# Kernel tuning notes

Measured on AMD Instinct MI355X. Metric: run time of the kernel, lower is better.

Reference implementation:

```python
import jax, jax.numpy as jnp
import numpy as np

N, S, IN_F, TEXT_D, EMB, H = 128, 1024, 768, 512, 512, 8
HD = EMB // H  # 64


def setup_inputs() -> dict:
    key = jax.random.key(0)
    ks = jax.random.split(key, 14)
    sc = 0.02
    return {
        "v": jax.random.normal(ks[0], (1, N, 12, IN_F), dtype=jnp.float32),
        "t": jax.random.normal(ks[1], (N, S, TEXT_D), dtype=jnp.float32),
        "t_len": jax.random.randint(ks[2], (N,), 1, S + 1, dtype=jnp.int32),
        "W_fc1": jax.random.normal(ks[3], (EMB, IN_F), dtype=jnp.float32) * sc,
        "b_fc1": jnp.zeros((EMB,), jnp.float32),
        "W_fc2": jax.random.normal(ks[4], (EMB, 12 * EMB), dtype=jnp.float32) * sc,
        "b_fc2": jnp.zeros((EMB,), jnp.float32),
        "Wq": jax.random.normal(ks[5], (EMB, EMB), dtype=jnp.float32) * sc,
        "Wk": jax.random.normal(ks[6], (EMB, TEXT_D), dtype=jnp.float32) * sc,
        "Wv": jax.random.normal(ks[7], (EMB, TEXT_D), dtype=jnp.float32) * sc,
        "bq": jnp.zeros((EMB,), jnp.float32),
        "bk": jnp.zeros((EMB,), jnp.float32),
        "bv": jnp.zeros((EMB,), jnp.float32),
        "Wo": jax.random.normal(ks[8], (EMB, EMB), dtype=jnp.float32) * sc,
        "bo": jnp.zeros((EMB,), jnp.float32),
    }


def reference(v, t, t_len, W_fc1, b_fc1, W_fc2, b_fc2, Wq, Wk, Wv, bq, bk, bv, Wo, bo):
    # fc1 + ReLU: [1,N,12,IN_F] -> [N,12,EMB]
    x = jax.nn.relu(jnp.einsum('onif,ef->onie', v, W_fc1) + b_fc1)[0]
    # flatten + fc2 + ReLU -> [N, EMB]
    x = x.reshape(N, 12 * EMB)
    vfeat = jax.nn.relu(x @ W_fc2.T + b_fc2)
    # Batched ragged multihead attention, query length 1 per item.
    scale = 1.0 / jnp.sqrt(jnp.asarray(HD, vfeat.dtype))
    q = ((vfeat @ Wq.T + bq) * scale).reshape(N, H, HD)           # [N,H,HD]
    k = (jnp.einsum('nsd,ed->nse', t, Wk) + bk).reshape(N, S, H, HD)
    vv = (jnp.einsum('nsd,ed->nse', t, Wv) + bv).reshape(N, S, H, HD)
    scores = jnp.einsum('nhd,nshd->nhs', q, k)                    # [N,H,S]
    valid = (jnp.arange(S)[None, :] < t_len[:, None])[:, None, :]  # [N,1,S]
    scores = jnp.where(valid, scores, jnp.finfo(scores.dtype).min)
    w = jax.nn.softmax(scores, axis=-1)                           # [N,H,S]
    ctx = jnp.einsum('nhs,nshd->nhd', w, vv).reshape(N, EMB)
    attn_out = ctx @ Wo.T + bo                                    # [N,EMB]
    return vfeat, attn_out
```

## Files before the change

### kernel.cpp

```cpp
#include <hip/hip_runtime.h>

#define NB 128
#define SSEQ 1024
#define TD 512
#define TSTR 516

typedef _Float16 half8 __attribute__((ext_vector_type(8)));
typedef _Float16 half4 __attribute__((ext_vector_type(4)));
typedef float f32x4 __attribute__((ext_vector_type(4)));

template<int AM, int BM>
__device__ __forceinline__ void gemm_body(
    const void* __restrict__ Av, int lda, long aSZ,
    const void* __restrict__ Bv, int ldb, long bSZ,
    const float* __restrict__ bias, const float* __restrict__ aRowScale,
    float scale, int doRelu, int outMode,
    float* __restrict__ outF, _Float16* __restrict__ outH,
    int ldc, int cColOff, int kTiles, long oSplit,
    int mt, int nt, int sp, int bz, int tid)
{
  __shared__ _Float16 As[64][72];
  __shared__ _Float16 Bs[64][72];
  int r = tid >> 2, kq = (tid & 3) * 16;
  int w = tid >> 6, l = tid & 63;
  long aoff = (long)bz * aSZ + (long)(mt * 64 + r) * lda + (long)sp * kTiles * 64 + kq;
  long boff = (long)bz * bSZ + (long)(nt * 64 + r) * ldb + (long)sp * kTiles * 64 + kq;
  const _Float16* apH = (const _Float16*)Av + aoff;
  const float*    apF = (const float*)Av + aoff;
  const _Float16* bpH = (const _Float16*)Bv + boff;
  const float*    bpF = (const float*)Bv + boff;
  float srA = 1.0f;
  if constexpr (AM == 2) srA = 1.0f / aRowScale[(mt * 64 + r) * 8 + bz];

  half8 pa0, pa1, pb0, pb1;
  f32x4 qa0, qa1, qa2, qa3, qc0, qc1, qc2, qc3;
  if constexpr (AM == 0) { pa0 = *(const half8*)apH; pa1 = *(const half8*)(apH + 8); }
  else { qa0 = *(const f32x4*)apF; qa1 = *(const f32x4*)(apF + 4);
         qa2 = *(const f32x4*)(apF + 8); qa3 = *(const f32x4*)(apF + 12); }
  if constexpr (BM == 0) { pb0 = *(const half8*)bpH; pb1 = *(const half8*)(bpH + 8); }
  else { qc0 = *(const f32x4*)bpF; qc1 = *(const f32x4*)(bpF + 4);
         qc2 = *(const f32x4*)(bpF + 8); qc3 = *(const f32x4*)(bpF + 12); }

  f32x4 acc[4];
  #pragma unroll
  for (int c = 0; c < 4; ++c) acc[c] = (f32x4){0.f, 0.f, 0.f, 0.f};
  int fr = l & 15, fo = (l >> 4) * 8;
  for (int kt = 0; kt < kTiles; ++kt) {
    __syncthreads();
    if constexpr (AM == 0) {
      *(half8*)&As[r][kq] = pa0; *(half8*)&As[r][kq + 8] = pa1;
    } else {
      f32x4 s0 = qa0, s1 = qa1, s2 = qa2, s3 = qa3;
      if constexpr (AM == 2) { s0 *= srA; s1 *= srA; s2 *= srA; s3 *= srA; }
      *(half4*)&As[r][kq + 0]  = __builtin_convertvector(s0, half4);
      *(half4*)&As[r][kq + 4]  = __builtin_convertvector(s1, half4);
      *(half4*)&As[r][kq + 8]  = __builtin_convertvector(s2, half4);
      *(half4*)&As[r][kq + 12] = __builtin_convertvector(s3, half4);
    }
    if constexpr (BM == 0) {
      *(half8*)&Bs[r][kq] = pb0; *(half8*)&Bs[r][kq + 8] = pb1;
    } else {
      *(half4*)&Bs[r][kq + 0]  = __builtin_convertvector(qc0, half4);
      *(half4*)&Bs[r][kq + 4]  = __builtin_convertvector(qc1, half4);
      *(half4*)&Bs[r][kq + 8]  = __builtin_convertvector(qc2, half4);
      *(half4*)&Bs[r][kq + 12] = __builtin_convertvector(qc3, half4);
    }
    __syncthreads();
    if (kt + 1 < kTiles) {
      apH += 64; apF += 64; bpH += 64; bpF += 64;
      if constexpr (AM == 0) { pa0 = *(const half8*)apH; pa1 = *(const half8*)(apH + 8); }
      else { qa0 = *(const f32x4*)apF; qa1 = *(const f32x4*)(apF + 4);
             qa2 = *(const f32x4*)(apF + 8); qa3 = *(const f32x4*)(apF + 12); }
      if constexpr (BM == 0) { pb0 = *(const half8*)bpH; pb1 = *(const half8*)(bpH + 8); }
      else { qc0 = *(const f32x4*)bpF; qc1 = *(const f32x4*)(bpF + 4);
             qc2 = *(const f32x4*)(bpF + 8); qc3 = *(const f32x4*)(bpF + 12); }
    }
    #pragma unroll
    for (int ks = 0; ks < 2; ++ks) {
      half8 af = *(const half8*)&As[16 * w + fr][ks * 32 + fo];
      #pragma unroll
      for (int c = 0; c < 4; ++c) {
        half8 bf = *(const half8*)&Bs[16 * c + fr][ks * 32 + fo];
        acc[c] = __builtin_amdgcn_mfma_f32_16x16x32_f16(af, bf, acc[c], 0, 0, 0);
      }
    }
  }
  int lrow = (l >> 4) * 4, lcol = l & 15;
  #pragma unroll
  for (int c = 0; c < 4; ++c) {
    #pragma unroll
    for (int rr = 0; rr < 4; ++rr) {
      int gm = mt * 64 + 16 * w + lrow + rr;
      int gn = nt * 64 + 16 * c + lcol;
      int ecol = gn + bz * cColOff;
      float vv = acc[c][rr];
      if (bias) vv += bias[ecol];
      vv *= scale;
      if (doRelu) vv = fmaxf(vv, 0.f);
      long oidx = (long)gm * ldc + ecol;
      if (outMode == 0) outF[oidx] = vv;
      else if (outMode == 1) outH[oidx] = (_Float16)vv;
      else outF[oidx + (long)sp * oSplit] = vv;
    }
  }
}

template<int AM, int BM>
__global__ __launch_bounds__(256) void k_gemm(
    const void* __restrict__ Av, int lda, long aSZ,
    const void* __restrict__ Bv, int ldb, long bSZ,
    const float* __restrict__ bias, const float* __restrict__ aRowScale,
    float scale, int doRelu, int outMode,
    float* __restrict__ outF, _Float16* __restrict__ outH,
    int ldc, int cColOff, int mtiles, int kTiles, long oSplit)
{
  gemm_body<AM, BM>(Av, lda, aSZ, Bv, ldb, bSZ, bias, aRowScale, scale, doRelu,
                    outMode, outF, outH, ldc, cColOff, kTiles, oSplit,
                    (int)blockIdx.x % mtiles, (int)blockIdx.x / mtiles,
                    (int)blockIdx.y, (int)blockIdx.z, (int)threadIdx.x);
}

__global__ __launch_bounds__(256) void k_prepfc1(
    const float* __restrict__ Wq, const float* __restrict__ Wk,
    const float* __restrict__ bq, const float* __restrict__ bk,
    _Float16* __restrict__ G16T, float* __restrict__ gb,
    float* __restrict__ qbc, float* __restrict__ cvec,
    float* __restrict__ pz, _Float16* __restrict__ qz,
    const float* __restrict__ v, const float* __restrict__ W1,
    const float* __restrict__ b1, _Float16* __restrict__ x16)
{
  int bx = blockIdx.x, tid = threadIdx.x;
  if (bx >= 512) {
    int s = bx - 512;
    gemm_body<1, 1>(v, 768, 0, W1, 768, 0, b1, nullptr, 1.f, 1, 1,
                    nullptr, x16, 512, 0, 12, 0, s % 24, s / 24, 0, 0, tid);
    return;
  }
  int b = bx;
  int gid = b * 256 + tid;
  for (long i = gid; i < 131328; i += 131072)
    *(f32x4*)(pz + 4 * i) = (f32x4){0.f, 0.f, 0.f, 0.f};
  {
    long i4 = (long)gid * 4;
    long n = i4 >> 12, off = i4 & 4095;
    *(half4*)(qz + n * 8192 + 4096 + off) = (half4){(_Float16)0, (_Float16)0, (_Float16)0, (_Float16)0};
  }
  int h = b >> 6, et = (b >> 3) & 7, dt = b & 7;
  __shared__ float Aq[64][68];
  __shared__ float Bk[64][68];
  __shared__ float bqs[64], bks[64];
  int r = tid >> 2, cq = (tid & 3) * 16;
  const float* wqp = Wq + (long)(h * 64 + r) * 512 + et * 64 + cq;
  const float* wkp = Wk + (long)(h * 64 + r) * 512 + dt * 64 + cq;
  #pragma unroll
  for (int c = 0; c < 4; ++c) {
    *(f32x4*)&Aq[r][cq + 4 * c] = *(const f32x4*)(wqp + 4 * c);
    *(f32x4*)&Bk[r][cq + 4 * c] = *(const f32x4*)(wkp + 4 * c);
  }
  if (tid < 64) { bqs[tid] = bq[h * 64 + tid]; bks[tid] = bk[h * 64 + tid]; }
  __syncthreads();
  int te = tid & 15, td = tid >> 4;
  float acc[4][4];
  #pragma unroll
  for (int a = 0; a < 4; ++a)
    #pragma unroll
    for (int d = 0; d < 4; ++d) acc[a][d] = 0.f;
  #pragma unroll 4
  for (int j = 0; j < 64; ++j) {
    f32x4 av = *(const f32x4*)&Aq[j][te * 4];
    f32x4 bv = *(const f32x4*)&Bk[j][td * 4];
    #pragma unroll
    for (int a = 0; a < 4; ++a)
      #pragma unroll
      for (int d = 0; d < 4; ++d) acc[a][d] = fmaf(av[a], bv[d], acc[a][d]);
  }
  #pragma unroll
  for (int d = 0; d < 4; ++d) {
    half4 hv = { (_Float16)(0.125f * acc[0][d]), (_Float16)(0.125f * acc[1][d]),
                 (_Float16)(0.125f * acc[2][d]), (_Float16)(0.125f * acc[3][d]) };
    *(half4*)(G16T + (long)h * 262144 + (long)(dt * 64 + td * 4 + d) * 512 + et * 64 + te * 4) = hv;
  }
  if (dt == 0 && td == 0) {
    #pragma unroll
    for (int i = 0; i < 4; ++i) {
      float s = 0.f;
      for (int j = 0; j < 64; ++j) s = fmaf(Aq[j][te * 4 + i], bks[j], s);
      gb[h * 512 + et * 64 + te * 4 + i] = 0.125f * s;
    }
  }
  if (et == 0 && te == 0) {
    #pragma unroll
    for (int i = 0; i < 4; ++i) {
      float s = 0.f;
      for (int j = 0; j < 64; ++j) s = fmaf(Bk[j][td * 4 + i], bqs[j], s);
      cvec[h * 512 + dt * 64 + td * 4 + i] = 0.125f * s;
    }
  }
  if (et == 0 && dt == 0 && tid == 0) {
    float s = 0.f;
    for (int j = 0; j < 64; ++j) s = fmaf(bqs[j], bks[j], s);
    qbc[h] = 0.125f * s;
  }
}

__global__ __launch_bounds__(256) void k_vfeat(
    const float* __restrict__ vacc, const float* __restrict__ b2,
    float* __restrict__ outF, _Float16* __restrict__ vf16)
{
  int i = blockIdx.x * 256 + threadIdx.x;
  float vv = b2[i & 511];
  #pragma unroll
  for (int sp = 0; sp < 16; ++sp) vv += vacc[sp * 65536 + i];
  vv = fmaxf(vv, 0.f);
  outF[i] = vv;
  vf16[i] = (_Float16)vv;
}

__global__ __launch_bounds__(256) void k_qkqb(
    const _Float16* __restrict__ vf16, const _Float16* __restrict__ G16T,
    const float* __restrict__ cvec, const float* __restrict__ gb,
    const float* __restrict__ qbc, _Float16* __restrict__ qk16,
    float* __restrict__ qb)
{
  int bx = blockIdx.x, tid = threadIdx.x;
  if (bx < 128) {
    int z = bx >> 4, s = bx & 15;
    gemm_body<0, 0>(vf16, 512, 0, G16T, 512, 262144, cvec, nullptr, 1.f, 0, 1,
                    nullptr, qk16, 8192, 512, 8, 0, s % 2, s / 2, 0, z, tid);
    return;
  }
  int n = bx - 128;
  __shared__ float qs[512];
  qs[tid] = (float)vf16[n * 512 + tid];
  qs[tid + 256] = (float)vf16[n * 512 + tid + 256];
  __syncthreads();
  int h = tid >> 5, j = tid & 31;
  float p = 0.f;
  for (int e = j; e < 512; e += 32) p = fmaf(qs[e], gb[h * 512 + e], p);
  #pragma unroll
  for (int m = 1; m < 32; m <<= 1) p += __shfl_xor(p, m, 32);
  if (j == 0) qb[n * 8 + h] = p + qbc[h];
}

__global__ __launch_bounds__(256) void k_attn(
    const float* __restrict__ t, const int* __restrict__ tlen,
    const _Float16* __restrict__ qk16, const float* __restrict__ qb,
    float* __restrict__ pu, float* __restrict__ pl)
{
  int n = blockIdx.x >> 4, j = blockIdx.x & 15;
  int len = tlen[n];
  int base = j * 64;
  if (base >= len) return;
  int s1 = base + 64; if (s1 > len) s1 = len;
  int tid = threadIdx.x, wid = tid >> 6, l = tid & 63;
  int fr = l & 15, fo = (l >> 4) * 8;

  __shared__ __align__(16) _Float16 ts[64][TSTR];
  __shared__ __align__(16) _Float16 wst[16][72];
  __shared__ float lred[8];
  if (tid < 8) lred[tid] = 0.f;

  const float* tn = t + (long)n * SSEQ * TD;
  {
    f32x4 a0, a1, b0, b1;
    auto ld = [&](int c, f32x4& x0, f32x4& x1) {
      int sg = base + c * 4 + wid;
      if (sg < s1) {
        const float* p = tn + (long)sg * TD;
        x0 = *(const f32x4*)(p + 4 * l);
        x1 = *(const f32x4*)(p + 256 + 4 * l);
      } else {
        x0 = (f32x4){0.f,0.f,0.f,0.f}; x1 = (f32x4){0.f,0.f,0.f,0.f};
      }
    };
    ld(0, a0, a1); ld(1, b0, b1);
    #pragma unroll
    for (int c = 0; c < 16; c += 2) {
      half4 h0 = __builtin_convertvector(a0, half4);
      half4 h1 = __builtin_convertvector(a1, half4);
      int row = c * 4 + wid;
      if (c + 2 < 16) ld(c + 2, a0, a1);
      *(half4*)&ts[row][4 * l] = h0;
      *(half4*)&ts[row][256 + 4 * l] = h1;
      half4 g0 = __builtin_convertvector(b0, half4);
      half4 g1 = __builtin_convertvector(b1, half4);
      int row2 = (c + 1) * 4 + wid;
      if (c + 3 < 16) ld(c + 3, b0, b1);
      *(half4*)&ts[row2][4 * l] = g0;
      *(half4*)&ts[row2][256 + 4 * l] = g1;
    }
  }
  __syncthreads();
  {
    const _Float16* qn = qk16 + (long)n * 8192 + fr * 512 + fo;
    f32x4 acc = (f32x4){0.f, 0.f, 0.f, 0.f};
    #pragma unroll 4
    for (int kt = 0; kt < 16; ++kt) {
      half8 bf = *(const half8*)(qn + kt * 32);
      const _Float16* ap = &ts[16 * wid + fr][kt * 32 + fo];
      half4 alo = *(const half4*)ap;
      half4 ahi = *(const half4*)(ap + 4);
      half8 af = { alo[0], alo[1], alo[2], alo[3], ahi[0], ahi[1], ahi[2], ahi[3] };
      acc = __builtin_amdgcn_mfma_f32_16x16x32_f16(af, bf, acc, 0, 0, 0);
    }
    float qbr = (fr < 8) ? qb[n * 8 + fr] : 0.f;
    float lac = 0.f;
    #pragma unroll
    for (int r = 0; r < 4; ++r) {
      int sl = 16 * wid + (l >> 4) * 4 + r;
      float wv = (fr < 8 && base + sl < s1) ? __expf(acc[r] + qbr) : 0.f;
      wst[fr][sl] = (_Float16)wv;
      lac += wv;
    }
    if (fr < 8) atomicAdd(&lred[fr], lac);
  }
  __syncthreads();
  f32x4 upv[8];
  #pragma unroll
  for (int dt = 0; dt < 8; ++dt) upv[dt] = (f32x4){0.f, 0.f, 0.f, 0.f};
  #pragma unroll
  for (int dt = 0; dt < 8; ++dt) {
    int dcol = 128 * wid + dt * 16 + fr;
    #pragma unroll
    for (int ks = 0; ks < 2; ++ks) {
      half8 af = *(const half8*)&wst[fr][ks * 32 + fo];
      half8 bf;
      #pragma unroll
      for (int jj = 0; jj < 8; ++jj) bf[jj] = ts[ks * 32 + fo + jj][dcol];
      upv[dt] = __builtin_amdgcn_mfma_f32_16x16x32_f16(af, bf, upv[dt], 0, 0, 0);
    }
  }
  int quad = l >> 4;
  float* pn = pu + (long)n * 4096;
  if (quad < 2) {
    #pragma unroll
    for (int dt = 0; dt < 8; ++dt) {
      int d = 128 * wid + dt * 16 + fr;
      #pragma unroll
      for (int r = 0; r < 4; ++r)
        atomicAdd(&pn[(quad * 4 + r) * 512 + d], upv[dt][r]);
    }
  }
  if (tid < 8) atomicAdd(&pl[n * 8 + tid], lred[tid]);
}

extern "C" void kernel_launch(void* const* d_in, const int* in_sizes, int n_in,
                              void* d_out, int out_size, void* d_ws, size_t ws_size,
                              hipStream_t stream)
{
  const float* v    = (const float*)d_in[0];
  const float* t    = (const float*)d_in[1];
  const int*   tlen = (const int*)d_in[2];
  const float* W1   = (const float*)d_in[3];
  const float* b1   = (const float*)d_in[4];
  const float* W2   = (const float*)d_in[5];
  const float* b2   = (const float*)d_in[6];
  const float* Wq   = (const float*)d_in[7];
  const float* Wk   = (const float*)d_in[8];
  const float* Wv   = (const float*)d_in[9];
  const float* bq   = (const float*)d_in[10];
  const float* bk   = (const float*)d_in[11];
  const float* bv   = (const float*)d_in[12];
  const float* Wo   = (const float*)d_in[13];
  const float* bo   = (const float*)d_in[14];
  float* out = (float*)d_out;

  _Float16* hb   = (_Float16*)d_ws;
  _Float16* x16  = hb;
  _Float16* vf16 = hb + 786432l;
  _Float16* ctx16= hb + 851968l;
  _Float16* qk16 = hb + 917504l;
  _Float16* G16T = hb + 1966080l;
  float* fb   = (float*)(hb + 4063232l);
  float* vacc = fb;
  float* pu   = fb + 1048576l;
  float* pl   = fb + 1572864l;
  float* qb   = fb + 1573888l;
  float* gb   = fb + 1574912l;
  float* qbc  = fb + 1579008l;
  float* cvec = fb + 1579024l;

  k_prepfc1<<<704, 256, 0, stream>>>(Wq, Wk, bq, bk, G16T, gb, qbc, cvec,
                                     pu, qk16, v, W1, b1, x16);
  k_gemm<0,1><<<dim3(16, 16, 1), 256, 0, stream>>>(x16, 6144, 0, W2, 6144, 0,
      nullptr, nullptr, 1.f, 0, 2, vacc, nullptr, 512, 0, 2, 6, 65536);
  k_vfeat<<<256, 256, 0, stream>>>(vacc, b2, out, vf16);
  k_qkqb<<<256, 256, 0, stream>>>(vf16, G16T, cvec, gb, qbc, qk16, qb);
  k_attn<<<NB * 16, 256, 0, stream>>>(t, tlen, qk16, qb, pu, pl);
  k_gemm<2,1><<<dim3(2, 1, 8), 256, 0, stream>>>(pu, 4096, 512, Wv, 512, 32768,
      bv, pl, 1.f, 0, 1, nullptr, ctx16, 512, 64, 2, 8, 0);
  k_gemm<0,1><<<dim3(16, 1, 1), 256, 0, stream>>>(ctx16, 512, 0, Wo, 512, 0,
      bo, nullptr, 1.f, 0, 0, out + 65536, nullptr, 512, 0, 2, 8, 0);
}
```

Baseline: 467.3 us.

## Fold Wv and Wo into one precomputed matrix and merge the output GEMMs

Precomputes M = Wo·Wv per head in the prep kernel, together with a folded bias, and replaces the two tail GEMMs (pu→ctx, ctx→out) with a single split-K GEMM that atomically accumulates into the zeroed output. The attention kernel also drops the shared-memory l reduction and a barrier, and adds s_setprio around its MFMA loops. This removes one launch and the ctx intermediate, in exchange for more prep work, atomic output accumulation and a changed rounding path for the projection.

New measurement: 476.5 us. No clear change (+2.0%).

```diff
diff --git a/kernel.cpp b/kernel.cpp
--- a/kernel.cpp
+++ b/kernel.cpp
@@ -30,7 +30,7 @@
   const _Float16* bpH = (const _Float16*)Bv + boff;
   const float*    bpF = (const float*)Bv + boff;
   float srA = 1.0f;
-  if constexpr (AM == 2) srA = 1.0f / aRowScale[(mt * 64 + r) * 8 + bz];
+  if constexpr (AM == 2) srA = 1.0f / aRowScale[(mt * 64 + r) * 8 + sp];
 
   half8 pa0, pa1, pb0, pb1;
   f32x4 qa0, qa1, qa2, qa3, qc0, qc1, qc2, qc3;
@@ -94,13 +94,14 @@
       int gn = nt * 64 + 16 * c + lcol;
       int ecol = gn + bz * cColOff;
       float vv = acc[c][rr];
-      if (bias) vv += bias[ecol];
+      if (bias && sp == 0) vv += bias[ecol];
       vv *= scale;
       if (doRelu) vv = fmaxf(vv, 0.f);
       long oidx = (long)gm * ldc + ecol;
       if (outMode == 0) outF[oidx] = vv;
       else if (outMode == 1) outH[oidx] = (_Float16)vv;
-      else outF[oidx + (long)sp * oSplit] = vv;
+      else if (outMode == 2) outF[oidx + (long)sp * oSplit] = vv;
+      else atomicAdd(&outF[oidx], vv);
     }
   }
 }
@@ -127,15 +128,76 @@
     float* __restrict__ qbc, float* __restrict__ cvec,
     float* __restrict__ pz, _Float16* __restrict__ qz,
     const float* __restrict__ v, const float* __restrict__ W1,
-    const float* __restrict__ b1, _Float16* __restrict__ x16)
+    const float* __restrict__ b1, _Float16* __restrict__ x16,
+    const float* __restrict__ Wv, const float* __restrict__ Wo,
+    const float* __restrict__ bv, _Float16* __restrict__ M16,
+    float* __restrict__ obo8)
 {
   int bx = blockIdx.x, tid = threadIdx.x;
-  if (bx >= 512) {
-    int s = bx - 512;
+  if (bx >= 1024) {
+    int s = bx - 1024;
     gemm_body<1, 1>(v, 768, 0, W1, 768, 0, b1, nullptr, 1.f, 1, 1,
                     nullptr, x16, 512, 0, 12, 0, s % 24, s / 24, 0, 0, tid);
     return;
   }
+  __shared__ float SA[64][68];
+  __shared__ float SB[64][68];
+  __shared__ float sv0[64], sv1[64];
+  int r = tid >> 2, cq = (tid & 3) * 16;
+  int te = tid & 15, td = tid >> 4;
+
+  if (bx >= 512) {
+    int b2 = bx - 512;
+    int h = b2 >> 6, et = (b2 >> 3) & 7, gt = b2 & 7;
+    const float* wvp = Wv + (long)(h * 64 + r) * 512 + gt * 64 + cq;
+    const float* wop = Wo + (long)(et * 64 + r) * 512 + h * 64 + cq;
+    #pragma unroll
+    for (int c = 0; c < 4; ++c)
+      *(f32x4*)&SA[r][cq + 4 * c] = *(const f32x4*)(wvp + 4 * c);
+    #pragma unroll
+    for (int c = 0; c < 4; ++c) {
+      f32x4 x = *(const f32x4*)(wop + 4 * c);
+      #pragma unroll
+      for (int i = 0; i < 4; ++i) SB[cq + 4 * c + i][r] = x[i];
+    }
+    if (tid < 64) sv0[tid] = bv[h * 64 + tid];
+    __syncthreads();
+    float acc[4][4];
+    #pragma unroll
+    for (int a = 0; a < 4; ++a)
+      #pragma unroll
+      for (int d = 0; d < 4; ++d) acc[a][d] = 0.f;
+    #pragma unroll 4
+    for (int jj = 0; jj < 64; ++jj) {
+      f32x4 av = *(const f32x4*)&SA[jj][te * 4];
+      f32x4 bt = *(const f32x4*)&SB[jj][td * 4];
+      #pragma unroll
+      for (int a = 0; a < 4; ++a)
+        #pragma unroll
+        for (int d = 0; d < 4; ++d) acc[a][d] = fmaf(av[a], bt[d], acc[a][d]);
+    }
+    #pragma unroll
+    for (int d = 0; d < 4; ++d) {
+      half4 hv = { (_Float16)acc[0][d], (_Float16)acc[1][d],
+                   (_Float16)acc[2][d], (_Float16)acc[3][d] };
+      *(half4*)(M16 + (long)(et * 64 + td * 4 + d) * 4096 + h * 512 + gt * 64 + te * 4) = hv;
+    }
+    if (gt == 0 && te == 0) {
+      float s0 = 0.f, s1 = 0.f, s2 = 0.f, s3 = 0.f;
+      for (int jj = 0; jj < 64; ++jj) {
+        f32x4 bt = *(const f32x4*)&SB[jj][td * 4];
+        float bb = sv0[jj];
+        s0 = fmaf(bt[0], bb, s0); s1 = fmaf(bt[1], bb, s1);
+        s2 = fmaf(bt[2], bb, s2); s3 = fmaf(bt[3], bb, s3);
+      }
+      obo8[h * 512 + et * 64 + td * 4 + 0] = s0;
+      obo8[h * 512 + et * 64 + td * 4 + 1] = s1;
+      obo8[h * 512 + et * 64 + td * 4 + 2] = s2;
+      obo8[h * 512 + et * 64 + td * 4 + 3] = s3;
+    }
+    return;
+  }
+
   int b = bx;
   int gid = b * 256 + tid;
   for (long i = gid; i < 131328; i += 131072)
@@ -146,20 +208,15 @@
     *(half4*)(qz + n * 8192 + 4096 + off) = (half4){(_Float16)0, (_Float16)0, (_Float16)0, (_Float16)0};
   }
   int h = b >> 6, et = (b >> 3) & 7, dt = b & 7;
-  __shared__ float Aq[64][68];
-  __shared__ float Bk[64][68];
-  __shared__ float bqs[64], bks[64];
-  int r = tid >> 2, cq = (tid & 3) * 16;
   const float* wqp = Wq + (long)(h * 64 + r) * 512 + et * 64 + cq;
   const float* wkp = Wk + (long)(h * 64 + r) * 512 + dt * 64 + cq;
   #pragma unroll
   for (int c = 0; c < 4; ++c) {
-    *(f32x4*)&Aq[r][cq + 4 * c] = *(const f32x4*)(wqp + 4 * c);
-    *(f32x4*)&Bk[r][cq + 4 * c] = *(const f32x4*)(wkp + 4 * c);
-  }
-  if (tid < 64) { bqs[tid] = bq[h * 64 + tid]; bks[tid] = bk[h * 64 + tid]; }
+    *(f32x4*)&SA[r][cq + 4 * c] = *(const f32x4*)(wqp + 4 * c);
+    *(f32x4*)&SB[r][cq + 4 * c] = *(const f32x4*)(wkp + 4 * c);
+  }
+  if (tid < 64) { sv0[tid] = bq[h * 64 + tid]; sv1[tid] = bk[h * 64 + tid]; }
   __syncthreads();
-  int te = tid & 15, td = tid >> 4;
   float acc[4][4];
   #pragma unroll
   for (int a = 0; a < 4; ++a)
@@ -167,12 +224,12 @@
     for (int d = 0; d < 4; ++d) acc[a][d] = 0.f;
   #pragma unroll 4
   for (int j = 0; j < 64; ++j) {
-    f32x4 av = *(const f32x4*)&Aq[j][te * 4];
-    f32x4 bv = *(const f32x4*)&Bk[j][td * 4];
+    f32x4 av = *(const f32x4*)&SA[j][te * 4];
+    f32x4 bv4 = *(const f32x4*)&SB[j][td * 4];
     #pragma unroll
     for (int a = 0; a < 4; ++a)
       #pragma unroll
-      for (int d = 0; d < 4; ++d) acc[a][d] = fmaf(av[a], bv[d], acc[a][d]);
+      for (int d = 0; d < 4; ++d) acc[a][d] = fmaf(av[a], bv4[d], acc[a][d]);
   }
   #pragma unroll
   for (int d = 0; d < 4; ++d) {
@@ -184,7 +241,7 @@
     #pragma unroll
     for (int i = 0; i < 4; ++i) {
       float s = 0.f;
-      for (int j = 0; j < 64; ++j) s = fmaf(Aq[j][te * 4 + i], bks[j], s);
+      for (int j = 0; j < 64; ++j) s = fmaf(SA[j][te * 4 + i], sv1[j], s);
       gb[h * 512 + et * 64 + te * 4 + i] = 0.125f * s;
     }
   }
@@ -192,20 +249,22 @@
     #pragma unroll
     for (int i = 0; i < 4; ++i) {
       float s = 0.f;
-      for (int j = 0; j < 64; ++j) s = fmaf(Bk[j][td * 4 + i], bqs[j], s);
+      for (int j = 0; j < 64; ++j) s = fmaf(SB[j][td * 4 + i], sv0[j], s);
       cvec[h * 512 + dt * 64 + td * 4 + i] = 0.125f * s;
     }
   }
   if (et == 0 && dt == 0 && tid == 0) {
     float s = 0.f;
-    for (int j = 0; j < 64; ++j) s = fmaf(bqs[j], bks[j], s);
+    for (int j = 0; j < 64; ++j) s = fmaf(sv0[j], sv1[j], s);
     qbc[h] = 0.125f * s;
   }
 }
 
 __global__ __launch_bounds__(256) void k_vfeat(
     const float* __restrict__ vacc, const float* __restrict__ b2,
-    float* __restrict__ outF, _Float16* __restrict__ vf16)
+    float* __restrict__ outF, _Float16* __restrict__ vf16,
+    const float* __restrict__ obo8, const float* __restrict__ bo,
+    float* __restrict__ obo)
 {
   int i = blockIdx.x * 256 + threadIdx.x;
   float vv = b2[i & 511];
@@ -214,13 +273,19 @@
   vv = fmaxf(vv, 0.f);
   outF[i] = vv;
   vf16[i] = (_Float16)vv;
+  if (i < 512) {
+    float s = bo[i];
+    #pragma unroll
+    for (int h = 0; h < 8; ++h) s += obo8[h * 512 + i];
+    obo[i] = s;
+  }
 }
 
 __global__ __launch_bounds__(256) void k_qkqb(
     const _Float16* __restrict__ vf16, const _Float16* __restrict__ G16T,
     const float* __restrict__ cvec, const float* __restrict__ gb,
     const float* __restrict__ qbc, _Float16* __restrict__ qk16,
-    float* __restrict__ qb)
+    float* __restrict__ qb, float* __restrict__ outz)
 {
   int bx = blockIdx.x, tid = threadIdx.x;
   if (bx < 128) {
@@ -230,6 +295,8 @@
     return;
   }
   int n = bx - 128;
+  float* oz = outz + (long)n * 512;
+  oz[tid] = 0.f; oz[tid + 256] = 0.f;
   __shared__ float qs[512];
   qs[tid] = (float)vf16[n * 512 + tid];
   qs[tid + 256] = (float)vf16[n * 512 + tid + 256];
@@ -257,14 +324,12 @@
 
   __shared__ __align__(16) _Float16 ts[64][TSTR];
   __shared__ __align__(16) _Float16 wst[16][72];
-  __shared__ float lred[8];
-  if (tid < 8) lred[tid] = 0.f;
 
   const float* tn = t + (long)n * SSEQ * TD;
   {
     f32x4 a0, a1, b0, b1;
-    auto ld = [&](int c, f32x4& x0, f32x4& x1) {
-      int sg = base + c * 4 + wid;
+    auto ld = [&](int rr, f32x4& x0, f32x4& x1) {
+      int sg = base + 16 * wid + rr;
       if (sg < s1) {
         const float* p = tn + (long)sg * TD;
         x0 = *(const f32x4*)(p + 4 * l);
@@ -275,25 +340,25 @@
     };
     ld(0, a0, a1); ld(1, b0, b1);
     #pragma unroll
-    for (int c = 0; c < 16; c += 2) {
+    for (int rr = 0; rr < 16; rr += 2) {
       half4 h0 = __builtin_convertvector(a0, half4);
       half4 h1 = __builtin_convertvector(a1, half4);
-      int row = c * 4 + wid;
-      if (c + 2 < 16) ld(c + 2, a0, a1);
+      int row = 16 * wid + rr;
+      if (rr + 2 < 16) ld(rr + 2, a0, a1);
       *(half4*)&ts[row][4 * l] = h0;
       *(half4*)&ts[row][256 + 4 * l] = h1;
       half4 g0 = __builtin_convertvector(b0, half4);
       half4 g1 = __builtin_convertvector(b1, half4);
-      int row2 = (c + 1) * 4 + wid;
-      if (c + 3 < 16) ld(c + 3, b0, b1);
-      *(half4*)&ts[row2][4 * l] = g0;
-      *(half4*)&ts[row2][256 + 4 * l] = g1;
-    }
-  }
-  __syncthreads();
+      if (rr + 3 < 16) ld(rr + 3, b0, b1);
+      *(half4*)&ts[row + 1][4 * l] = g0;
+      *(half4*)&ts[row + 1][256 + 4 * l] = g1;
+    }
+  }
   {
     const _Float16* qn = qk16 + (long)n * 8192 + fr * 512 + fo;
+    float qbr = (fr < 8) ? qb[n * 8 + fr] : 0.f;
     f32x4 acc = (f32x4){0.f, 0.f, 0.f, 0.f};
+    __builtin_amdgcn_s_setprio(1);
     #pragma unroll 4
     for (int kt = 0; kt < 16; ++kt) {
       half8 bf = *(const half8*)(qn + kt * 32);
@@ -303,7 +368,7 @@
       half8 af = { alo[0], alo[1], alo[2], alo[3], ahi[0], ahi[1], ahi[2], ahi[3] };
       acc = __builtin_amdgcn_mfma_f32_16x16x32_f16(af, bf, acc, 0, 0, 0);
     }
-    float qbr = (fr < 8) ? qb[n * 8 + fr] : 0.f;
+    __builtin_amdgcn_s_setprio(0);
     float lac = 0.f;
     #pragma unroll
     for (int r = 0; r < 4; ++r) {
@@ -312,12 +377,13 @@
       wst[fr][sl] = (_Float16)wv;
       lac += wv;
     }
-    if (fr < 8) atomicAdd(&lred[fr], lac);
+    if (fr < 8) atomicAdd(&pl[n * 8 + fr], lac);
   }
   __syncthreads();
   f32x4 upv[8];
   #pragma unroll
   for (int dt = 0; dt < 8; ++dt) upv[dt] = (f32x4){0.f, 0.f, 0.f, 0.f};
+  __builtin_amdgcn_s_setprio(1);
   #pragma unroll
   for (int dt = 0; dt < 8; ++dt) {
     int dcol = 128 * wid + dt * 16 + fr;
@@ -330,6 +396,7 @@
       upv[dt] = __builtin_amdgcn_mfma_f32_16x16x32_f16(af, bf, upv[dt], 0, 0, 0);
     }
   }
+  __builtin_amdgcn_s_setprio(0);
   int quad = l >> 4;
   float* pn = pu + (long)n * 4096;
   if (quad < 2) {
@@ -341,7 +408,6 @@
         atomicAdd(&pn[(quad * 4 + r) * 512 + d], upv[dt][r]);
     }
   }
-  if (tid < 8) atomicAdd(&pl[n * 8 + tid], lred[tid]);
 }
 
 extern "C" void kernel_launch(void* const* d_in, const int* in_sizes, int n_in,
@@ -368,10 +434,10 @@
   _Float16* hb   = (_Float16*)d_ws;
   _Float16* x16  = hb;
   _Float16* vf16 = hb + 786432l;
-  _Float16* ctx16= hb + 851968l;
-  _Float16* qk16 = hb + 917504l;
-  _Float16* G16T = hb + 1966080l;
-  float* fb   = (float*)(hb + 4063232l);
+  _Float16* qk16 = hb + 851968l;
+  _Float16* G16T = hb + 1900544l;
+  _Float16* M16  = hb + 3997696l;
+  float* fb   = (float*)(hb + 6094848l);
   float* vacc = fb;
   float* pu   = fb + 1048576l;
   float* pl   = fb + 1572864l;
@@ -379,16 +445,16 @@
   float* gb   = fb + 1574912l;
   float* qbc  = fb + 1579008l;
   float* cvec = fb + 1579024l;
-
-  k_prepfc1<<<704, 256, 0, stream>>>(Wq, Wk, bq, bk, G16T, gb, qbc, cvec,
-                                     pu, qk16, v, W1, b1, x16);
+  float* obo8 = fb + 1583120l;
+  float* obo  = fb + 1587216l;
+
+  k_prepfc1<<<1216, 256, 0, stream>>>(Wq, Wk, bq, bk, G16T, gb, qbc, cvec,
+                                      pu, qk16, v, W1, b1, x16, Wv, Wo, bv, M16, obo8);
   k_gemm<0,1><<<dim3(16, 16, 1), 256, 0, stream>>>(x16, 6144, 0, W2, 6144, 0,
       nullptr, nullptr, 1.f, 0, 2, vacc, nullptr, 512, 0, 2, 6, 65536);
-  k_vfeat<<<256, 256, 0, stream>>>(vacc, b2, out, vf16);
-  k_qkqb<<<256, 256, 0, stream>>>(vf16, G16T, cvec, gb, qbc, qk16, qb);
+  k_vfeat<<<256, 256, 0, stream>>>(vacc, b2, out, vf16, obo8, bo, obo);
+  k_qkqb<<<256, 256, 0, stream>>>(vf16, G16T, cvec, gb, qbc, qk16, qb, out + 65536);
   k_attn<<<NB * 16, 256, 0, stream>>>(t, tlen, qk16, qb, pu, pl);
-  k_gemm<2,1><<<dim3(2, 1, 8), 256, 0, stream>>>(pu, 4096, 512, Wv, 512, 32768,
-      bv, pl, 1.f, 0, 1, nullptr, ctx16, 512, 64, 2, 8, 0);
-  k_gemm<0,1><<<dim3(16, 1, 1), 256, 0, stream>>>(ctx16, 512, 0, Wo, 512, 0,
-      bo, nullptr, 1.f, 0, 0, out + 65536, nullptr, 512, 0, 2, 8, 0);
-}
+  k_gemm<2,0><<<dim3(16, 8, 1), 256, 0, stream>>>(pu, 4096, 0, M16, 4096, 0,
+      obo, pl, 1.f, 0, 3, out + 65536, nullptr, 512, 0, 2, 8, 0);
+}
```
